# Kernel optimization log

Measured on AMD Instinct MI355X. Metric: run time of the kernel, lower is better.

## Reference

```python
import jax, jax.numpy as jnp
import numpy as np

N = 500000      # num_edges
D = 128         # embedding_dim
S = 256         # num_samples (negatives)
TEMPERATURE = 0.1
EPS_NORM = 1e-12  # torch F.normalize eps
EPS_COS = 1e-8    # torch F.cosine_similarity eps


def setup_inputs() -> dict:
    key = jax.random.key(0)
    k1, k2, k3 = jax.random.split(key, 3)
    edge_embeddings = jax.random.normal(k1, (N, D), dtype=jnp.float32)
    positive_indices = jax.random.randint(k2, (N,), 0, N, dtype=jnp.int64)
    negative_indices = jax.random.randint(k3, (S,), 0, N, dtype=jnp.int64)
    return {
        "edge_embeddings": edge_embeddings,
        "positive_indices": positive_indices,
        "negative_indices": negative_indices,
    }


def _l2_normalize(x, eps):
    # matches torch: x / max(||x||_2, eps)
    n = jnp.sqrt(jnp.sum(x * x, axis=-1, keepdims=True))
    return x / jnp.maximum(n, eps)


def reference(edge_embeddings, positive_indices, negative_indices):
    # Normalize once; positives reuse the same per-row normalization.
    norm_all = _l2_normalize(edge_embeddings, EPS_NORM)          # [N, D]
    pos_norm = norm_all[positive_indices]                         # [N, D]
    positive_sim = jnp.sum(norm_all * pos_norm, axis=-1)          # [N]

    # cosine_similarity uses eps=1e-8 denominator clamp
    norm_all_cos = _l2_normalize(edge_embeddings, EPS_COS)        # [N, D]
    neg_norm = norm_all_cos[negative_indices]                     # [S, D]
    negative_sim = jnp.einsum('nd,sd->ns', norm_all_cos, neg_norm)  # [N, S]

    positive_logit = positive_sim / TEMPERATURE                   # [N]
    negative_logit = negative_sim / TEMPERATURE                   # [N, S]
    negative = jax.nn.logsumexp(negative_logit, axis=1) - jnp.log(jnp.float32(S))
    loss = -jnp.mean(positive_logit - negative)
    return loss
```

## Files before the change

kernel.cpp:

```cpp
#include <hip/hip_runtime.h>
#include <hip/hip_bf16.h>
#include <math.h>

#define D 128
#define S 256
#define ROWS 64
#define LOG_S 5.545177444479562f

typedef __attribute__((ext_vector_type(8)))  short    short8;
typedef __attribute__((ext_vector_type(8)))  __bf16   bf16x8;
typedef __attribute__((ext_vector_type(16))) float    floatx16;

typedef const __attribute__((address_space(1))) void gas_void;
typedef __attribute__((address_space(3))) void las_void;

__device__ __forceinline__ unsigned short f2bf(float x) {
  __hip_bfloat16 h = __float2bfloat16(x);
  return *(unsigned short*)&h;
}

__global__ void neg_norm_kernel(const float* __restrict__ emb,
                                const int* __restrict__ negidx,
                                unsigned short* __restrict__ negsw) {
  int s = blockIdx.x;
  int L = threadIdx.x;
  long idx = (long)negidx[s];
  float2 v = *(const float2*)(emb + idx * D + L * 2);
  float ss = v.x * v.x + v.y * v.y;
#pragma unroll
  for (int off = 1; off < 64; off <<= 1) ss += __shfl_xor(ss, off);
  float sc = 10.0f / fmaxf(sqrtf(ss), 1e-8f);
  int chunk = s >> 7, nr = s & 127;
  int lu = L >> 2, pos = (L & 3) * 2;
  int u = lu ^ (nr & 15);
  ushort2 o = make_ushort2(f2bf(v.x * sc), f2bf(v.y * sc));
  *(ushort2*)(negsw + chunk * 16384 + nr * 128 + u * 8 + pos) = o;
}

__global__ __launch_bounds__(256, 3)
void hyper_main(const float* __restrict__ emb,
                const int* __restrict__ posidx,
                const unsigned short* __restrict__ negsw,
                double* __restrict__ acc,
                int N) {
  __shared__ __align__(16) char smem[49152];
  unsigned short* rows_l = (unsigned short*)smem;
  unsigned short* negs_l = (unsigned short*)(smem + 16384);

  const int t = threadIdx.x;
  const int lane = t & 63;
  const int w = t >> 6;
  const long rbase = (long)blockIdx.x * ROWS;

  {
    const char* g = (const char*)negsw + w * 8192 + lane * 16;
    char* l = (char*)negs_l + w * 8192;
#pragma unroll
    for (int i = 0; i < 8; ++i)
      __builtin_amdgcn_global_load_lds((gas_void*)(g + i * 1024),
                                       (las_void*)(l + i * 1024), 16, 0, 0);
  }

  const int r  = t >> 2;
  const int qq = t & 3;
  long n = rbase + r;
  bool valid = (n < (long)N);
  long pi = 0;
  if (valid) pi = (long)posidx[n];

  float4 v[8];
  float ssv = 0.f, ssp = 0.f, dp = 0.f;
#pragma unroll
  for (int k = 0; k < 8; ++k) {
    int c4 = qq + 4 * k;
    float4 vv = make_float4(0.f, 0.f, 0.f, 0.f);
    float4 pp = make_float4(0.f, 0.f, 0.f, 0.f);
    if (valid) {
      vv = *(const float4*)(emb + n * D + c4 * 4);
      pp = *(const float4*)(emb + pi * D + c4 * 4);
    }
    v[k] = vv;
    ssv += vv.x*vv.x + vv.y*vv.y + vv.z*vv.z + vv.w*vv.w;
    ssp += pp.x*pp.x + pp.y*pp.y + pp.z*pp.z + pp.w*pp.w;
    dp  += vv.x*pp.x + vv.y*pp.y + vv.z*pp.z + vv.w*pp.w;
  }
#pragma unroll
  for (int off = 1; off < 4; off <<= 1) {
    ssv += __shfl_xor(ssv, off);
    ssp += __shfl_xor(ssp, off);
    dp  += __shfl_xor(dp,  off);
  }
  float inv8 = 1.0f / fmaxf(sqrtf(ssv), 1e-8f);
#pragma unroll
  for (int k = 0; k < 8; ++k) {
    int c4 = qq + 4 * k;
    int u = (c4 >> 1) ^ (r & 15);
    ushort4 o = make_ushort4(f2bf(v[k].x*inv8), f2bf(v[k].y*inv8),
                             f2bf(v[k].z*inv8), f2bf(v[k].w*inv8));
    *(ushort4*)&rows_l[r * 128 + u * 8 + (c4 & 1) * 4] = o;
  }
  float possum = 0.f;
  if (qq == 0 && valid) {
    float invv = 1.0f / fmaxf(sqrtf(ssv), 1e-12f);
    float invp = 1.0f / fmaxf(sqrtf(ssp), 1e-12f);
    possum = dp * invv * invp * 10.0f;
  }

  const int q   = lane >> 5;
  const int ln  = lane & 31;
  const int tr  = w >> 1;
  const int chh = w & 1;
  const int arow  = tr * 32 + ln;
  const int nrow0 = chh * 64 + ln;
  const int nrow1 = nrow0 + 32;

  float se[16];
#pragma unroll
  for (int i = 0; i < 16; ++i) se[i] = 0.f;

  for (int c = 0; c < 2; ++c) {
    __syncthreads();
    floatx16 acc0 = {};
    floatx16 acc1 = {};
#pragma unroll
    for (int ki = 0; ki < 8; ++ki) {
      int lu = ki * 2 + q;
      short8 a  = *(const short8*)&rows_l[arow  * 128 + (lu ^ (arow  & 15)) * 8];
      short8 b0 = *(const short8*)&negs_l[nrow0 * 128 + (lu ^ (nrow0 & 15)) * 8];
      short8 b1 = *(const short8*)&negs_l[nrow1 * 128 + (lu ^ (nrow1 & 15)) * 8];
      acc0 = __builtin_amdgcn_mfma_f32_32x32x16_bf16(
          __builtin_bit_cast(bf16x8, a), __builtin_bit_cast(bf16x8, b0), acc0, 0, 0, 0);
      acc1 = __builtin_amdgcn_mfma_f32_32x32x16_bf16(
          __builtin_bit_cast(bf16x8, a), __builtin_bit_cast(bf16x8, b1), acc1, 0, 0, 0);
    }
    if (c == 0) {
      __syncthreads();
      const char* g = (const char*)negsw + 32768 + w * 8192 + lane * 16;
      char* l = (char*)negs_l + w * 8192;
#pragma unroll
      for (int i = 0; i < 8; ++i)
        __builtin_amdgcn_global_load_lds((gas_void*)(g + i * 1024),
                                         (las_void*)(l + i * 1024), 16, 0, 0);
    }
#pragma unroll
    for (int rg = 0; rg < 16; ++rg)
      se[rg] += __expf(acc0[rg]) + __expf(acc1[rg]);
  }

#pragma unroll
  for (int rg = 0; rg < 16; ++rg) {
    float sv = se[rg];
#pragma unroll
    for (int off = 1; off < 32; off <<= 1) sv += __shfl_xor(sv, off);
    se[rg] = sv;
  }

  __syncthreads();
  float* sebuf = (float*)smem;
  if (ln == 0) {
#pragma unroll
    for (int rg = 0; rg < 16; ++rg) {
      int rr = tr * 32 + (rg & 3) + 8 * (rg >> 2) + 4 * q;
      sebuf[rr * 2 + chh] = se[rg];
    }
  }
  __syncthreads();

  float negterm = 0.f;
  if (t < 64) {
    long n2 = rbase + t;
    if (n2 < (long)N)
      negterm = __logf(sebuf[t * 2] + sebuf[t * 2 + 1]) - LOG_S;
  }

  float local = negterm - possum;
#pragma unroll
  for (int off = 1; off < 64; off <<= 1) local += __shfl_xor(local, off);
  float* red = (float*)(smem + 2048);
  if (lane == 0) red[w] = local;
  __syncthreads();
  if (t == 0) {
    double tot = (double)red[0] + (double)red[1] +
                 (double)red[2] + (double)red[3];
    atomicAdd(acc, tot);
  }
}

__global__ void finish_kernel(const double* __restrict__ acc,
                              float* __restrict__ out, int N) {
  out[0] = (float)(acc[0] / (double)N);
}

extern "C" void kernel_launch(void* const* d_in, const int* in_sizes, int n_in,
                              void* d_out, int out_size, void* d_ws, size_t ws_size,
                              hipStream_t stream) {
  const float* emb  = (const float*)d_in[0];
  const int* posidx = (const int*)d_in[1];
  const int* negidx = (const int*)d_in[2];
  int N = in_sizes[1];

  double* acc = (double*)d_ws;
  unsigned short* negsw = (unsigned short*)((char*)d_ws + 256);

  hipMemsetAsync(d_ws, 0, 256, stream);
  neg_norm_kernel<<<S, 64, 0, stream>>>(emb, negidx, negsw);
  int grid = (N + ROWS - 1) / ROWS;
  hyper_main<<<grid, 256, 0, stream>>>(emb, posidx, negsw, acc, N);
  finish_kernel<<<1, 1, 0, stream>>>(acc, (float*)d_out, N);
}
```

Before: 411.2 us.

## Read negatives directly from global in MFMA-fragment layout, cut LDS for occupancy

Rewrites the negative-embedding buffer into a layout where each lane's MFMA B fragment is a contiguous 16-byte chunk, so the main kernel loads fragments straight from global (L2-resident) memory instead of staging 32KB through LDS. This removes the per-block global-to-LDS copies and the barriers tied to them, shrinks shared memory to 16KB, and raises the launch-bounds occupancy target from 3 to 6 blocks. The trade-off is that every block now issues repeated global/L2 reads for the negatives, and the higher occupancy target may cost registers.

Result: slower. 494.3 us (+20.2%).

```diff
diff --git a/kernel.cpp b/kernel.cpp
--- a/kernel.cpp
+++ b/kernel.cpp
@@ -10,9 +10,6 @@
 typedef __attribute__((ext_vector_type(8)))  short    short8;
 typedef __attribute__((ext_vector_type(8)))  __bf16   bf16x8;
 typedef __attribute__((ext_vector_type(16))) float    floatx16;
-
-typedef const __attribute__((address_space(1))) void gas_void;
-typedef __attribute__((address_space(3))) void las_void;
 
 __device__ __forceinline__ unsigned short f2bf(float x) {
   __hip_bfloat16 h = __float2bfloat16(x);
@@ -30,36 +27,26 @@
 #pragma unroll
   for (int off = 1; off < 64; off <<= 1) ss += __shfl_xor(ss, off);
   float sc = 10.0f / fmaxf(sqrtf(ss), 1e-8f);
-  int chunk = s >> 7, nr = s & 127;
-  int lu = L >> 2, pos = (L & 3) * 2;
-  int u = lu ^ (nr & 15);
+  int g = s >> 5, c = s & 31;
+  int k0 = 2 * L;
+  int ki = k0 >> 4, h = (k0 >> 3) & 1, j = k0 & 7;
   ushort2 o = make_ushort2(f2bf(v.x * sc), f2bf(v.y * sc));
-  *(ushort2*)(negsw + chunk * 16384 + nr * 128 + u * 8 + pos) = o;
+  *(ushort2*)(negsw + (size_t)((g * 8 + ki) * 64 + h * 32 + c) * 8 + j) = o;
 }
 
-__global__ __launch_bounds__(256, 3)
+__global__ __launch_bounds__(256, 6)
 void hyper_main(const float* __restrict__ emb,
                 const int* __restrict__ posidx,
                 const unsigned short* __restrict__ negsw,
                 double* __restrict__ acc,
                 int N) {
-  __shared__ __align__(16) char smem[49152];
+  __shared__ __align__(16) char smem[16384];
   unsigned short* rows_l = (unsigned short*)smem;
-  unsigned short* negs_l = (unsigned short*)(smem + 16384);
 
   const int t = threadIdx.x;
   const int lane = t & 63;
   const int w = t >> 6;
   const long rbase = (long)blockIdx.x * ROWS;
-
-  {
-    const char* g = (const char*)negsw + w * 8192 + lane * 16;
-    char* l = (char*)negs_l + w * 8192;
-#pragma unroll
-    for (int i = 0; i < 8; ++i)
-      __builtin_amdgcn_global_load_lds((gas_void*)(g + i * 1024),
-                                       (las_void*)(l + i * 1024), 16, 0, 0);
-  }
 
   const int r  = t >> 2;
   const int qq = t & 3;
@@ -110,37 +97,29 @@
   const int ln  = lane & 31;
   const int tr  = w >> 1;
   const int chh = w & 1;
-  const int arow  = tr * 32 + ln;
-  const int nrow0 = chh * 64 + ln;
-  const int nrow1 = nrow0 + 32;
+  const int arow = tr * 32 + ln;
 
   float se[16];
 #pragma unroll
   for (int i = 0; i < 16; ++i) se[i] = 0.f;
 
+  __syncthreads();
+
+#pragma unroll 1
   for (int c = 0; c < 2; ++c) {
-    __syncthreads();
+    const int gA = chh * 4 + c * 2;
     floatx16 acc0 = {};
     floatx16 acc1 = {};
 #pragma unroll
     for (int ki = 0; ki < 8; ++ki) {
       int lu = ki * 2 + q;
-      short8 a  = *(const short8*)&rows_l[arow  * 128 + (lu ^ (arow  & 15)) * 8];
-      short8 b0 = *(const short8*)&negs_l[nrow0 * 128 + (lu ^ (nrow0 & 15)) * 8];
-      short8 b1 = *(const short8*)&negs_l[nrow1 * 128 + (lu ^ (nrow1 & 15)) * 8];
+      short8 a  = *(const short8*)&rows_l[arow * 128 + (lu ^ (arow & 15)) * 8];
+      short8 b0 = *(const short8*)(negsw + (size_t)(((gA    ) * 8 + ki) * 64 + lane) * 8);
+      short8 b1 = *(const short8*)(negsw + (size_t)(((gA + 1) * 8 + ki) * 64 + lane) * 8);
       acc0 = __builtin_amdgcn_mfma_f32_32x32x16_bf16(
           __builtin_bit_cast(bf16x8, a), __builtin_bit_cast(bf16x8, b0), acc0, 0, 0, 0);
       acc1 = __builtin_amdgcn_mfma_f32_32x32x16_bf16(
           __builtin_bit_cast(bf16x8, a), __builtin_bit_cast(bf16x8, b1), acc1, 0, 0, 0);
-    }
-    if (c == 0) {
-      __syncthreads();
-      const char* g = (const char*)negsw + 32768 + w * 8192 + lane * 16;
-      char* l = (char*)negs_l + w * 8192;
-#pragma unroll
-      for (int i = 0; i < 8; ++i)
-        __builtin_amdgcn_global_load_lds((gas_void*)(g + i * 1024),
-                                         (las_void*)(l + i * 1024), 16, 0, 0);
     }
 #pragma unroll
     for (int rg = 0; rg < 16; ++rg)
```
